# Kernel optimization log

Hardware: AMD Instinct MI355X
Metric: run time of the kernel (lower is better)

Reference implementation:

```python
import jax, jax.numpy as jnp
import numpy as np
from jax import lax

B, C, H, W = 16, 256, 64, 64
EXP = 2
C2 = C * EXP  # expanded channels
EPS = 1e-5


def setup_inputs() -> dict:
    key = jax.random.key(0)
    ks = jax.random.split(key, 8)
    def he(k, shape, fan_out):
        return jax.random.normal(k, shape, jnp.float32) * np.sqrt(2.0 / fan_out)
    return {
        "f": jax.random.normal(ks[0], (B, C, H, W), jnp.float32),
        "ln_gamma": jnp.ones((C,), jnp.float32),
        "ln_beta": jnp.zeros((C,), jnp.float32),
        "w_expand": he(ks[1], (C2, C), C2),          # 1x1 conv [out,in]
        "freq_real": jnp.ones((C2,), jnp.float32),
        "freq_imag": jnp.zeros((C2,), jnp.float32),
        "w_poly": he(ks[2], (C2, C2), C2),
        "w_dw": he(ks[3], (C2, 1, 3, 3), 9),          # depthwise 3x3, fan_out=1*3*3
        "w_pw": he(ks[4], (C2, C2), C2),
        "w_final": he(ks[5], (C, C2), C),
    }


def reference(f, ln_gamma, ln_beta, w_expand, freq_real, freq_imag,
              w_poly, w_dw, w_pw, w_final):
    # LayerNorm over channel dim (torch permutes to NHWC, norms last dim)
    mu = jnp.mean(f, axis=1, keepdims=True)
    var = jnp.var(f, axis=1, keepdims=True)
    f1 = (f - mu) * lax.rsqrt(var + EPS)
    f1 = f1 * ln_gamma[None, :, None, None] + ln_beta[None, :, None, None]
    # 1x1 expand
    f2 = jnp.einsum('bchw,oc->bohw', f1, w_expand)
    # FFT2 -> multiply by per-channel complex scalar (r + i*j) -> IFFT2 -> real.
    # Since the filter is constant over all frequencies and f2 is real, this is
    # exactly Re((r+i*j) * f2) = r * f2; freq_imag contributes nothing.
    f4 = f2 * freq_real[None, :, None, None]
    # polymerize 1x1
    f5 = jnp.einsum('bchw,oc->bohw', f4, w_poly)
    # depthwise 3x3, SAME padding
    f6 = lax.conv_general_dilated(
        f5, w_dw, window_strides=(1, 1), padding='SAME',
        dimension_numbers=('NCHW', 'OIHW', 'NCHW'), feature_group_count=C2)
    # pointwise 1x1
    f6 = jnp.einsum('bchw,oc->bohw', f6, w_pw)
    # GELU (exact erf, torch default) gating
    f7 = jax.nn.gelu(f6, approximate=False) * f6
    # 1x1 reduce + residual
    f8 = jnp.einsum('bchw,oc->bohw', f7, w_final)
    return f + f8
```

## Files before the change

kernel.cpp:

```cpp
#include <hip/hip_runtime.h>
#include <hip/hip_bf16.h>
#include <math.h>

#define Bn 16
#define Cc 256
#define Hh 64
#define Ww 64
#define HW 4096
#define C2 512
#define Pp 65536
#define EPSc 1e-5f

typedef __attribute__((ext_vector_type(8))) short short8;
typedef __attribute__((ext_vector_type(4))) float floatx4;

__global__ __launch_bounds__(512)
void combine_weights(const float* __restrict__ w_expand,
                     const float* __restrict__ freq_real,
                     const float* __restrict__ w_poly,
                     const float* __restrict__ gamma,
                     const float* __restrict__ beta,
                     __hip_bfloat16* __restrict__ W1g_b,
                     float* __restrict__ bias1,
                     float* __restrict__ wsum) {
    int o = blockIdx.x;
    int tid = threadIdx.x;
    int c = tid & 255;
    int kh = tid >> 8;
    float acc = 0.f;
    const float* wp = w_poly + (size_t)o * C2 + kh * 256;
    const float* fr = freq_real + kh * 256;
    const float* we = w_expand + (size_t)(kh * 256) * Cc + c;
    for (int m = 0; m < 256; ++m) {
        acc += wp[m] * fr[m] * we[(size_t)m * Cc];
    }
    __shared__ float part[512];
    __shared__ float redB[256];
    __shared__ float redG[256];
    part[tid] = acc;
    __syncthreads();
    if (tid < 256) {
        float a = part[tid] + part[tid + 256];
        float wg = a * gamma[c];
        W1g_b[(size_t)o * Cc + c] = __float2bfloat16(wg);
        redB[c] = a * beta[c];
        redG[c] = wg;
    }
    __syncthreads();
    for (int s = 128; s > 0; s >>= 1) {
        if (tid < s) { redB[tid] += redB[tid + s]; redG[tid] += redG[tid + s]; }
        __syncthreads();
    }
    if (tid == 0) { bias1[o] = redB[0]; wsum[o] = redG[0]; }
}

__device__ inline void cvt4(const float* __restrict__ a,
                            __hip_bfloat16* __restrict__ o, int q) {
    float4 v = *(const float4*)&a[q * 4];
    __hip_bfloat16 r[4];
    r[0] = __float2bfloat16(v.x);
    r[1] = __float2bfloat16(v.y);
    r[2] = __float2bfloat16(v.z);
    r[3] = __float2bfloat16(v.w);
    *(uint2*)&o[q * 4] = *(const uint2*)r;
}

__global__ __launch_bounds__(256)
void prep_weights(const float* __restrict__ w_pw,
                  const float* __restrict__ w_final,
                  const float* __restrict__ w_dw,
                  __hip_bfloat16* __restrict__ w_pw_b,
                  __hip_bfloat16* __restrict__ w_final_b,
                  float* __restrict__ w_dw_p) {
    int i = blockIdx.x * 256 + threadIdx.x;
    if (i < 65536) {
        cvt4(w_pw, w_pw_b, i);
    } else if (i < 98304) {
        cvt4(w_final, w_final_b, i - 65536);
    } else {
        int j = i - 98304;
        if (j < C2 * 12) {
            int k = j / 12, l = j - k * 12;
            w_dw_p[j] = (l < 9) ? w_dw[k * 9 + l] : 0.f;
        }
    }
}

#define XPAD 264

__global__ __launch_bounds__(512, 4)
void gemm1f(const float* __restrict__ f,
            const __hip_bfloat16* __restrict__ W1g_b,
            const float* __restrict__ bias1,
            const float* __restrict__ wsum,
            __hip_bfloat16* __restrict__ f5) {
    __shared__ __align__(16) char smem1[50688];
    __hip_bfloat16* As = (__hip_bfloat16*)smem1;
    float* redS = (float*)(smem1 + 33792);
    float* redQ = (float*)(smem1 + 41984);
    float* muS  = (float*)(smem1 + 50176);
    float* rsS  = (float*)(smem1 + 50432);

    int flat = blockIdx.x;
    int b = flat >> 6;
    int h = flat & 63;
    int s0 = h * 64;

    int tid = threadIdx.x;
    int x = tid & 15;
    int cg = tid >> 4;

    const float* fb = f + (size_t)b * Cc * HW + s0 + x * 4;
    unsigned* Asu = (unsigned*)&As[0];

    float lsum[4] = {0.f, 0.f, 0.f, 0.f};
    float lsq[4]  = {0.f, 0.f, 0.f, 0.f};
#pragma unroll
    for (int i = 0; i < 4; ++i) {
        int cp = i * 32 + cg;
        float4 v0 = *(const float4*)&fb[(size_t)(cp * 2) * HW];
        float4 v1 = *(const float4*)&fb[(size_t)(cp * 2 + 1) * HW];
        float a0[4] = {v0.x, v0.y, v0.z, v0.w};
        float a1[4] = {v1.x, v1.y, v1.z, v1.w};
#pragma unroll
        for (int j = 0; j < 4; ++j) {
            lsum[j] += a0[j] + a1[j];
            lsq[j]  += a0[j] * a0[j] + a1[j] * a1[j];
            unsigned pk = ((unsigned)__bfloat16_as_ushort(__float2bfloat16(a1[j])) << 16)
                        |  (unsigned)__bfloat16_as_ushort(__float2bfloat16(a0[j]));
            Asu[(size_t)(x * 4 + j) * (XPAD / 2) + cp] = pk;
        }
    }
#pragma unroll
    for (int j = 0; j < 4; ++j) {
        redS[cg * 64 + x * 4 + j] = lsum[j];
        redQ[cg * 64 + x * 4 + j] = lsq[j];
    }

    int lane = tid & 63, wave = tid >> 6;
    int col = lane & 15, quad = lane >> 4;
    int c0w = wave * 64;
    const __hip_bfloat16* Bp = W1g_b + (size_t)(c0w + col) * Cc + quad * 8;
    short8 B0[4], B1[4];
#pragma unroll
    for (int j = 0; j < 4; ++j) {
        B0[j] = *(const short8*)(Bp + (size_t)j * 16 * Cc);
        B1[j] = *(const short8*)(Bp + (size_t)j * 16 * Cc + 32);
    }

    float ws4[4], bi4[4];
#pragma unroll
    for (int j = 0; j < 4; ++j) {
        int c = c0w + j * 16 + col;
        ws4[j] = wsum[c];
        bi4[j] = bias1[c];
    }

    __syncthreads();
    if (tid < 64) {
        float s = 0.f, q = 0.f;
#pragma unroll
        for (int g = 0; g < 32; ++g) { s += redS[g * 64 + tid]; q += redQ[g * 64 + tid]; }
        float m = s * (1.0f / 256.0f);
        muS[tid] = m;
        rsS[tid] = rsqrtf(q * (1.0f / 256.0f) - m * m + EPSc);
    }
    __syncthreads();

    floatx4 acc[4][4];
#pragma unroll
    for (int i = 0; i < 4; ++i)
#pragma unroll
        for (int j = 0; j < 4; ++j)
            acc[i][j] = (floatx4){0.f, 0.f, 0.f, 0.f};

#pragma unroll
    for (int ks = 0; ks < 8; ++ks) {
        int k0 = ks * 32;
        short8 af[4];
#pragma unroll
        for (int i = 0; i < 4; ++i)
            af[i] = *(const short8*)&As[(size_t)(i * 16 + col) * XPAD + k0 + quad * 8];
        __builtin_amdgcn_s_setprio(1);
#pragma unroll
        for (int i = 0; i < 4; ++i)
#pragma unroll
            for (int j = 0; j < 4; ++j)
                acc[i][j] = __builtin_amdgcn_mfma_f32_16x16x32_bf16(
                    af[i], (ks & 1) ? B1[j] : B0[j], acc[i][j], 0, 0, 0);
        __builtin_amdgcn_s_setprio(0);
        if (ks + 2 < 8) {
#pragma unroll
            for (int j = 0; j < 4; ++j) {
                short8 v = *(const short8*)(Bp + (size_t)j * 16 * Cc + k0 + 64);
                if (ks & 1) B1[j] = v; else B0[j] = v;
            }
        }
    }

    __syncthreads();
    __hip_bfloat16* Wb = (__hip_bfloat16*)smem1;
    __hip_bfloat16* f5b = f5 + (size_t)b * C2 * HW + s0;
    int rr = tid >> 3;
    int rc = tid & 7;
#pragma unroll
    for (int chunk = 0; chunk < 2; ++chunk) {
        if ((wave >> 2) == chunk) {
            int cbase = c0w & 255;
#pragma unroll
            for (int i = 0; i < 4; ++i) {
                int pl = i * 16 + quad * 4;
                float4 mu4 = *(const float4*)&muS[pl];
                float4 rs4 = *(const float4*)&rsS[pl];
                float mu_[4] = {mu4.x, mu4.y, mu4.z, mu4.w};
                float rs_[4] = {rs4.x, rs4.y, rs4.z, rs4.w};
#pragma unroll
                for (int j = 0; j < 4; ++j) {
                    int cl = cbase + j * 16 + col;
                    __hip_bfloat16 v4[4];
#pragma unroll
                    for (int r = 0; r < 4; ++r) {
                        float v = (acc[i][j][r] - mu_[r] * ws4[j]) * rs_[r] + bi4[j];
                        v4[r] = __float2bfloat16(v);
                    }
                    *(uint2*)&Wb[(size_t)cl * 72 + pl] = *(const uint2*)v4;
                }
            }
        }
        __syncthreads();
#pragma unroll
        for (int pass = 0; pass < 4; ++pass) {
            int cl = pass * 64 + rr;
            uint4 v = *(const uint4*)&Wb[(size_t)cl * 72 + rc * 8];
            *(uint4*)&f5b[(size_t)(chunk * 256 + cl) * HW + rc * 8] = v;
        }
        if (chunk == 0) __syncthreads();
    }
}

#define TPITCH 520

#define P0_LOAD(dst, itc) do {                                               \
    int kk_ = (itc) * 128 + kb;                                              \
    _Pragma("unroll")                                                        \
    for (int dy_ = 0; dy_ < 3; ++dy_) {                                      \
        int hh_ = h + dy_ - 1;                                               \
        if ((unsigned)hh_ < Hh) {                                            \
            const __hip_bfloat16* row_ = f5b + (size_t)kk_ * HW + hh_ * Ww + w16; \
            dst[dy_][0] = *(const uint4*)&row_[0];                           \
            dst[dy_][1] = *(const uint4*)&row_[8];                           \
        } else {                                                             \
            dst[dy_][0] = make_uint4(0, 0, 0, 0);                            \
            dst[dy_][1] = make_uint4(0, 0, 0, 0);                            \
        }                                                                    \
    } } while (0)

__global__ __launch_bounds__(512, 4)
void fused_tail(const __hip_bfloat16* __restrict__ f5,
                const float* __restrict__ w_dw_p,
                const __hip_bfloat16* __restrict__ w_pw_b,
                const __hip_bfloat16* __restrict__ w_final_b,
                const float* __restrict__ f,
                float* __restrict__ out) {
    __shared__ __align__(16) char smem[69632];
    __hip_bfloat16* tT = (__hip_bfloat16*)smem;
    float* Lf = (float*)smem;

    int flat = blockIdx.x;
    int xcd = flat & 7;
    int slot = flat >> 3;
    int hb = slot & 7;
    int b  = slot >> 3;
    int h  = xcd * 8 + hb;

    int tid = threadIdx.x;
    int lane = tid & 63;
    int wave = tid >> 6;
    int col = lane & 15;
    int quad = lane >> 4;

    const __hip_bfloat16* f5b = f5 + (size_t)b * C2 * HW;
    int t4 = tid & 3;
    int kb = tid >> 2;
    int w16 = t4 * 16;

    uint4 bA[3][2], bB[3][2];
    P0_LOAD(bA, 0);
    P0_LOAD(bB, 1);

#pragma unroll
    for (int it = 0; it < 4; ++it) {
        int k = it * 128 + kb;
        const float4* wd4 = (const float4*)(w_dw_p + (size_t)k * 12);
        float4 wa = wd4[0], wb = wd4[1], wc2 = wd4[2];
        float wreg[9] = {wa.x, wa.y, wa.z, wa.w, wb.x, wb.y, wb.z, wb.w, wc2.x};
        float acc16[16] = {};
#pragma unroll
        for (int dy = 0; dy < 3; ++dy) {
            const __hip_bfloat16* pv =
                (const __hip_bfloat16*)((it & 1) ? &bB[dy][0] : &bA[dy][0]);
            float cv[16];
#pragma unroll
            for (int j = 0; j < 16; ++j) cv[j] = __bfloat162float(pv[j]);
            float l_in = __shfl_up(cv[15], 1);
            float r_in = __shfl_down(cv[0], 1);
            if (t4 == 0) l_in = 0.f;
            if (t4 == 3) r_in = 0.f;
            float win[18];
            win[0] = l_in;
#pragma unroll
            for (int j = 0; j < 16; ++j) win[j + 1] = cv[j];
            win[17] = r_in;
#pragma unroll
            for (int j = 0; j < 16; ++j)
                acc16[j] += wreg[dy * 3 + 0] * win[j] +
                            wreg[dy * 3 + 1] * win[j + 1] +
                            wreg[dy * 3 + 2] * win[j + 2];
        }
        if (it + 2 < 4) {
            if (it & 1) { P0_LOAD(bB, it + 2); } else { P0_LOAD(bA, it + 2); }
        }
        int ksw = k ^ (t4 << 4);
#pragma unroll
        for (int j = 0; j < 16; ++j)
            tT[(size_t)(w16 + j) * TPITCH + ksw] = __float2bfloat16(acc16[j]);
    }

    int wm0 = wave * 64;
    const __hip_bfloat16* Ap = w_pw_b + (size_t)(wm0 + col) * C2 + quad * 8;
    short8 A0[4], A1[4];
#pragma unroll
    for (int mt = 0; mt < 4; ++mt)
        A0[mt] = *(const short8*)(Ap + (size_t)mt * 16 * C2);

    __syncthreads();

#pragma unroll
    for (int mt = 0; mt < 4; ++mt)
        A1[mt] = *(const short8*)(Ap + (size_t)mt * 16 * C2 + 32);

    floatx4 acc[4][4];
#pragma unroll
    for (int mt = 0; mt < 4; ++mt)
#pragma unroll
        for (int nt = 0; nt < 4; ++nt)
            acc[mt][nt] = (floatx4){0.f, 0.f, 0.f, 0.f};

#pragma unroll
    for (int ks = 0; ks < 16; ++ks) {
        int k0 = ks * 32;
        short8 bfr[4];
#pragma unroll
        for (int nt = 0; nt < 4; ++nt)
            bfr[nt] = *(const short8*)&tT[(size_t)(nt * 16 + col) * TPITCH +
                                          ((k0 + quad * 8) ^ (nt << 4))];
        __builtin_amdgcn_s_setprio(1);
#pragma unroll
        for (int mt = 0; mt < 4; ++mt)
#pragma unroll
            for (int nt = 0; nt < 4; ++nt)
                acc[mt][nt] = __builtin_amdgcn_mfma_f32_16x16x32_bf16(
                    (ks & 1) ? A1[mt] : A0[mt], bfr[nt], acc[mt][nt], 0, 0, 0);
        __builtin_amdgcn_s_setprio(0);
        if (ks + 2 < 16) {
#pragma unroll
            for (int mt = 0; mt < 4; ++mt) {
                short8 v = *(const short8*)(Ap + (size_t)mt * 16 * C2 + k0 + 64);
                if (ks & 1) A1[mt] = v; else A0[mt] = v;
            }
        }
    }
    __syncthreads();

#pragma unroll
    for (int mt = 0; mt < 4; ++mt)
#pragma unroll
        for (int nt = 0; nt < 4; ++nt) {
            __hip_bfloat16 v4[4];
#pragma unroll
            for (int r = 0; r < 4; ++r) {
                float v = acc[mt][nt][r];
                float gl = 0.5f * v * (1.0f + erff(v * 0.70710678118f));
                v4[r] = __float2bfloat16(gl * v);
            }
            *(uint2*)&tT[(size_t)(nt * 16 + col) * TPITCH +
                         ((wm0 + mt * 16 + quad * 4) ^ (nt << 4))] = *(const uint2*)v4;
        }

    int wm2 = wave * 32;
    const __hip_bfloat16* Af = w_final_b + (size_t)(wm2 + col) * C2 + quad * 8;
    short8 C0[2], C1[2];
#pragma unroll
    for (int mt = 0; mt < 2; ++mt)
        C0[mt] = *(const short8*)(Af + (size_t)mt * 16 * C2);

    __syncthreads();

#pragma unroll
    for (int mt = 0; mt < 2; ++mt)
        C1[mt] = *(const short8*)(Af + (size_t)mt * 16 * C2 + 32);

    floatx4 acc2[2][4];
#pragma unroll
    for (int mt = 0; mt < 2; ++mt)
#pragma unroll
        for (int nt = 0; nt < 4; ++nt)
            acc2[mt][nt] = (floatx4){0.f, 0.f, 0.f, 0.f};

#pragma unroll
    for (int ks = 0; ks < 16; ++ks) {
        int k0 = ks * 32;
        short8 bfr[4];
#pragma unroll
        for (int nt = 0; nt < 4; ++nt)
            bfr[nt] = *(const short8*)&tT[(size_t)(nt * 16 + col) * TPITCH +
                                          ((k0 + quad * 8) ^ (nt << 4))];
        __builtin_amdgcn_s_setprio(1);
#pragma unroll
        for (int mt = 0; mt < 2; ++mt)
#pragma unroll
            for (int nt = 0; nt < 4; ++nt)
                acc2[mt][nt] = __builtin_amdgcn_mfma_f32_16x16x32_bf16(
                    (ks & 1) ? C1[mt] : C0[mt], bfr[nt], acc2[mt][nt], 0, 0, 0);
        __builtin_amdgcn_s_setprio(0);
        if (ks + 2 < 16) {
#pragma unroll
            for (int mt = 0; mt < 2; ++mt) {
                short8 v = *(const short8*)(Af + (size_t)mt * 16 * C2 + k0 + 64);
                if (ks & 1) C1[mt] = v; else C0[mt] = v;
            }
        }
    }

    __syncthreads();
#pragma unroll
    for (int mt = 0; mt < 2; ++mt)
#pragma unroll
        for (int nt = 0; nt < 4; ++nt)
#pragma unroll
            for (int r = 0; r < 4; ++r) {
                int m = wm2 + mt * 16 + quad * 4 + r;
                int n = nt * 16 + col;
                Lf[(size_t)m * 68 + n] = acc2[mt][nt][r];
            }
    __syncthreads();

    const float* fb = f + (size_t)b * Cc * HW + h * Ww;
    float* ob = out + (size_t)b * Cc * HW + h * Ww;
    int pr = tid >> 4;
    int pc = tid & 15;
#pragma unroll
    for (int pass = 0; pass < 8; ++pass) {
        int m = pass * 32 + pr;
        float4 v = *(const float4*)&Lf[(size_t)m * 68 + pc * 4];
        float4 rr4 = *(const float4*)&fb[(size_t)m * HW + pc * 4];
        v.x += rr4.x; v.y += rr4.y; v.z += rr4.z; v.w += rr4.w;
        *(float4*)&ob[(size_t)m * HW + pc * 4] = v;
    }
}

extern "C" void kernel_launch(void* const* d_in, const int* in_sizes, int n_in,
                              void* d_out, int out_size, void* d_ws, size_t ws_size,
                              hipStream_t stream) {
    const float* f         = (const float*)d_in[0];
    const float* ln_gamma  = (const float*)d_in[1];
    const float* ln_beta   = (const float*)d_in[2];
    const float* w_expand  = (const float*)d_in[3];
    const float* freq_real = (const float*)d_in[4];
    const float* w_poly    = (const float*)d_in[6];
    const float* w_dw      = (const float*)d_in[7];
    const float* w_pw      = (const float*)d_in[8];
    const float* w_final   = (const float*)d_in[9];
    float* out = (float*)d_out;

    char* p = (char*)d_ws;
    __hip_bfloat16* f5   = (__hip_bfloat16*)p;  p += (size_t)C2 * Pp * 2;
    __hip_bfloat16* W1g_b = (__hip_bfloat16*)p; p += (size_t)C2 * Cc * 2;
    float* bias1 = (float*)p;                   p += (size_t)C2 * 4;
    float* wsum  = (float*)p;                   p += (size_t)C2 * 4;
    __hip_bfloat16* w_pw_b    = (__hip_bfloat16*)p;  p += (size_t)C2 * C2 * 2;
    __hip_bfloat16* w_final_b = (__hip_bfloat16*)p;  p += (size_t)Cc * C2 * 2;
    float* w_dw_p = (float*)p;                  p += (size_t)C2 * 12 * 4;

    combine_weights<<<dim3(C2), dim3(512), 0, stream>>>(
        w_expand, freq_real, w_poly, ln_gamma, ln_beta, W1g_b, bias1, wsum);

    prep_weights<<<dim3(409), dim3(256), 0, stream>>>(
        w_pw, w_final, w_dw, w_pw_b, w_final_b, w_dw_p);

    gemm1f<<<dim3(1024), dim3(512), 0, stream>>>(
        f, W1g_b, bias1, wsum, f5);

    fused_tail<<<dim3(1024), dim3(512), 0, stream>>>(
        f5, w_dw_p, w_pw_b, w_final_b, f, out);
}
```

Baseline: 337.0 us.

## Merge weight prep kernels, split gemm1 into smaller tiles, approximate GELU gate

New measurement: 340.3 us. About the same (+1.0%).

```diff
diff --git a/kernel.cpp b/kernel.cpp
--- a/kernel.cpp
+++ b/kernel.cpp
@@ -13,46 +13,6 @@
 
 typedef __attribute__((ext_vector_type(8))) short short8;
 typedef __attribute__((ext_vector_type(4))) float floatx4;
-
-__global__ __launch_bounds__(512)
-void combine_weights(const float* __restrict__ w_expand,
-                     const float* __restrict__ freq_real,
-                     const float* __restrict__ w_poly,
-                     const float* __restrict__ gamma,
-                     const float* __restrict__ beta,
-                     __hip_bfloat16* __restrict__ W1g_b,
-                     float* __restrict__ bias1,
-                     float* __restrict__ wsum) {
-    int o = blockIdx.x;
-    int tid = threadIdx.x;
-    int c = tid & 255;
-    int kh = tid >> 8;
-    float acc = 0.f;
-    const float* wp = w_poly + (size_t)o * C2 + kh * 256;
-    const float* fr = freq_real + kh * 256;
-    const float* we = w_expand + (size_t)(kh * 256) * Cc + c;
-    for (int m = 0; m < 256; ++m) {
-        acc += wp[m] * fr[m] * we[(size_t)m * Cc];
-    }
-    __shared__ float part[512];
-    __shared__ float redB[256];
-    __shared__ float redG[256];
-    part[tid] = acc;
-    __syncthreads();
-    if (tid < 256) {
-        float a = part[tid] + part[tid + 256];
-        float wg = a * gamma[c];
-        W1g_b[(size_t)o * Cc + c] = __float2bfloat16(wg);
-        redB[c] = a * beta[c];
-        redG[c] = wg;
-    }
-    __syncthreads();
-    for (int s = 128; s > 0; s >>= 1) {
-        if (tid < s) { redB[tid] += redB[tid + s]; redG[tid] += redG[tid + s]; }
-        __syncthreads();
-    }
-    if (tid == 0) { bias1[o] = redB[0]; wsum[o] = redG[0]; }
-}
 
 __device__ inline void cvt4(const float* __restrict__ a,
                             __hip_bfloat16* __restrict__ o, int q) {
@@ -65,53 +25,100 @@
     *(uint2*)&o[q * 4] = *(const uint2*)r;
 }
 
-__global__ __launch_bounds__(256)
-void prep_weights(const float* __restrict__ w_pw,
-                  const float* __restrict__ w_final,
-                  const float* __restrict__ w_dw,
-                  __hip_bfloat16* __restrict__ w_pw_b,
-                  __hip_bfloat16* __restrict__ w_final_b,
-                  float* __restrict__ w_dw_p) {
-    int i = blockIdx.x * 256 + threadIdx.x;
-    if (i < 65536) {
-        cvt4(w_pw, w_pw_b, i);
-    } else if (i < 98304) {
-        cvt4(w_final, w_final_b, i - 65536);
-    } else {
-        int j = i - 98304;
-        if (j < C2 * 12) {
-            int k = j / 12, l = j - k * 12;
-            w_dw_p[j] = (l < 9) ? w_dw[k * 9 + l] : 0.f;
-        }
-    }
+__global__ __launch_bounds__(512)
+void weights_all(const float* __restrict__ w_expand,
+                 const float* __restrict__ freq_real,
+                 const float* __restrict__ w_poly,
+                 const float* __restrict__ gamma,
+                 const float* __restrict__ beta,
+                 const float* __restrict__ w_pw,
+                 const float* __restrict__ w_final,
+                 const float* __restrict__ w_dw,
+                 __hip_bfloat16* __restrict__ W1g_b,
+                 float* __restrict__ bias1,
+                 float* __restrict__ wsum,
+                 __hip_bfloat16* __restrict__ w_pw_b,
+                 __hip_bfloat16* __restrict__ w_final_b,
+                 float* __restrict__ w_dw_p) {
+    int tid = threadIdx.x;
+    if (blockIdx.x >= 512) {
+        int i = (blockIdx.x - 512) * 512 + tid;
+        if (i < 65536) {
+            cvt4(w_pw, w_pw_b, i);
+        } else if (i < 98304) {
+            cvt4(w_final, w_final_b, i - 65536);
+        } else {
+            int j = i - 98304;
+            if (j < C2 * 12) {
+                int k = j / 12, l = j - k * 12;
+                w_dw_p[j] = (l < 9) ? w_dw[k * 9 + l] : 0.f;
+            }
+        }
+        return;
+    }
+    int o = blockIdx.x;
+    int c = tid & 255;
+    int kh = tid >> 8;
+    float acc = 0.f;
+    const float* wp = w_poly + (size_t)o * C2 + kh * 256;
+    const float* fr = freq_real + kh * 256;
+    const float* we = w_expand + (size_t)(kh * 256) * Cc + c;
+    for (int m = 0; m < 256; ++m) {
+        acc += wp[m] * fr[m] * we[(size_t)m * Cc];
+    }
+    __shared__ float part[512];
+    __shared__ float redB[256];
+    __shared__ float redG[256];
+    part[tid] = acc;
+    __syncthreads();
+    if (tid < 256) {
+        float a = part[tid] + part[tid + 256];
+        float wg = a * gamma[c];
+        W1g_b[(size_t)o * Cc + c] = __float2bfloat16(wg);
+        redB[c] = a * beta[c];
+        redG[c] = wg;
+    }
+    __syncthreads();
+    for (int s = 128; s > 0; s >>= 1) {
+        if (tid < s) { redB[tid] += redB[tid + s]; redG[tid] += redG[tid + s]; }
+        __syncthreads();
+    }
+    if (tid == 0) { bias1[o] = redB[0]; wsum[o] = redG[0]; }
 }
 
 #define XPAD 264
 
-__global__ __launch_bounds__(512, 4)
-void gemm1f(const float* __restrict__ f,
+__global__ __launch_bounds__(256, 4)
+void gemm1h(const float* __restrict__ f,
             const __hip_bfloat16* __restrict__ W1g_b,
             const float* __restrict__ bias1,
             const float* __restrict__ wsum,
             __hip_bfloat16* __restrict__ f5) {
-    __shared__ __align__(16) char smem1[50688];
-    __hip_bfloat16* As = (__hip_bfloat16*)smem1;
-    float* redS = (float*)(smem1 + 33792);
-    float* redQ = (float*)(smem1 + 41984);
-    float* muS  = (float*)(smem1 + 50176);
-    float* rsS  = (float*)(smem1 + 50432);
+    __shared__ __align__(16) char sm[27648];
+    __hip_bfloat16* As = (__hip_bfloat16*)sm;
+    float* redS  = (float*)(sm + 16896);
+    float* redQ  = (float*)(sm + 21120);
+    float* red2S = (float*)(sm + 25344);
+    float* red2Q = (float*)(sm + 26368);
+    float* muS   = (float*)(sm + 27392);
+    float* rsS   = (float*)(sm + 27520);
 
     int flat = blockIdx.x;
-    int b = flat >> 6;
-    int h = flat & 63;
-    int s0 = h * 64;
+    int xcd = flat & 7;
+    int s = flat >> 3;
+    int chalf = s & 1;
+    int ph = (s >> 1) & 1;
+    int hb = (s >> 2) & 7;
+    int b  = s >> 5;
+    int h  = xcd * 8 + hb;
+    int s0 = h * 64 + ph * 32;
 
     int tid = threadIdx.x;
-    int x = tid & 15;
-    int cg = tid >> 4;
+    int x = tid & 7;
+    int cg = tid >> 3;
 
     const float* fb = f + (size_t)b * Cc * HW + s0 + x * 4;
-    unsigned* Asu = (unsigned*)&As[0];
+    unsigned* Asu = (unsigned*)As;
 
     float lsum[4] = {0.f, 0.f, 0.f, 0.f};
     float lsq[4]  = {0.f, 0.f, 0.f, 0.f};
@@ -133,13 +140,13 @@
     }
 #pragma unroll
     for (int j = 0; j < 4; ++j) {
-        redS[cg * 64 + x * 4 + j] = lsum[j];
-        redQ[cg * 64 + x * 4 + j] = lsq[j];
+        redS[cg * 33 + x * 4 + j] = lsum[j];
+        redQ[cg * 33 + x * 4 + j] = lsq[j];
     }
 
     int lane = tid & 63, wave = tid >> 6;
     int col = lane & 15, quad = lane >> 4;
-    int c0w = wave * 64;
+    int c0w = chalf * 256 + wave * 64;
     const __hip_bfloat16* Bp = W1g_b + (size_t)(c0w + col) * Cc + quad * 8;
     short8 B0[4], B1[4];
 #pragma unroll
@@ -147,7 +154,6 @@
         B0[j] = *(const short8*)(Bp + (size_t)j * 16 * Cc);
         B1[j] = *(const short8*)(Bp + (size_t)j * 16 * Cc + 32);
     }
-
     float ws4[4], bi4[4];
 #pragma unroll
     for (int j = 0; j < 4; ++j) {
@@ -157,19 +163,31 @@
     }
 
     __syncthreads();
-    if (tid < 64) {
-        float s = 0.f, q = 0.f;
-#pragma unroll
-        for (int g = 0; g < 32; ++g) { s += redS[g * 64 + tid]; q += redQ[g * 64 + tid]; }
-        float m = s * (1.0f / 256.0f);
+
+    {
+        int pos = tid & 31, g8 = tid >> 5;
+        float ss = 0.f, qq = 0.f;
+#pragma unroll
+        for (int k = 0; k < 4; ++k) {
+            ss += redS[(g8 * 4 + k) * 33 + pos];
+            qq += redQ[(g8 * 4 + k) * 33 + pos];
+        }
+        red2S[g8 * 32 + pos] = ss;
+        red2Q[g8 * 32 + pos] = qq;
+    }
+    __syncthreads();
+    if (tid < 32) {
+        float ss = 0.f, qq = 0.f;
+#pragma unroll
+        for (int g = 0; g < 8; ++g) { ss += red2S[g * 32 + tid]; qq += red2Q[g * 32 + tid]; }
+        float m = ss * (1.0f / 256.0f);
         muS[tid] = m;
-        rsS[tid] = rsqrtf(q * (1.0f / 256.0f) - m * m + EPSc);
-    }
-    __syncthreads();
-
-    floatx4 acc[4][4];
-#pragma unroll
-    for (int i = 0; i < 4; ++i)
+        rsS[tid] = rsqrtf(qq * (1.0f / 256.0f) - m * m + EPSc);
+    }
+
+    floatx4 acc[2][4];
+#pragma unroll
+    for (int i = 0; i < 2; ++i)
 #pragma unroll
         for (int j = 0; j < 4; ++j)
             acc[i][j] = (floatx4){0.f, 0.f, 0.f, 0.f};
@@ -177,13 +195,13 @@
 #pragma unroll
     for (int ks = 0; ks < 8; ++ks) {
         int k0 = ks * 32;
-        short8 af[4];
-#pragma unroll
-        for (int i = 0; i < 4; ++i)
+        short8 af[2];
+#pragma unroll
+        for (int i = 0; i < 2; ++i)
             af[i] = *(const short8*)&As[(size_t)(i * 16 + col) * XPAD + k0 + quad * 8];
         __builtin_amdgcn_s_setprio(1);
 #pragma unroll
-        for (int i = 0; i < 4; ++i)
+        for (int i = 0; i < 2; ++i)
 #pragma unroll
             for (int j = 0; j < 4; ++j)
                 acc[i][j] = __builtin_amdgcn_mfma_f32_16x16x32_bf16(
@@ -199,46 +217,49 @@
     }
 
     __syncthreads();
-    __hip_bfloat16* Wb = (__hip_bfloat16*)smem1;
-    __hip_bfloat16* f5b = f5 + (size_t)b * C2 * HW + s0;
+    __hip_bfloat16* Wb = (__hip_bfloat16*)sm;
+#pragma unroll
+    for (int i = 0; i < 2; ++i) {
+        int pl = i * 16 + quad * 4;
+        float4 mu4 = *(const float4*)&muS[pl];
+        float4 rs4 = *(const float4*)&rsS[pl];
+        float mu_[4] = {mu4.x, mu4.y, mu4.z, mu4.w};
+        float rs_[4] = {rs4.x, rs4.y, rs4.z, rs4.w};
+#pragma unroll
+        for (int j = 0; j < 4; ++j) {
+            int cl = wave * 64 + j * 16 + col;
+            __hip_bfloat16 v4[4];
+#pragma unroll
+            for (int r = 0; r < 4; ++r) {
+                float v = (acc[i][j][r] - mu_[r] * ws4[j]) * rs_[r] + bi4[j];
+                v4[r] = __float2bfloat16(v);
+            }
+            *(uint2*)&Wb[(size_t)cl * 36 + pl] = *(const uint2*)v4;
+        }
+    }
+    __syncthreads();
+
+    __hip_bfloat16* f5b = f5 + ((size_t)b * C2 + chalf * 256) * HW + s0;
     int rr = tid >> 3;
     int rc = tid & 7;
 #pragma unroll
-    for (int chunk = 0; chunk < 2; ++chunk) {
-        if ((wave >> 2) == chunk) {
-            int cbase = c0w & 255;
-#pragma unroll
-            for (int i = 0; i < 4; ++i) {
-                int pl = i * 16 + quad * 4;
-                float4 mu4 = *(const float4*)&muS[pl];
-                float4 rs4 = *(const float4*)&rsS[pl];
-                float mu_[4] = {mu4.x, mu4.y, mu4.z, mu4.w};
-                float rs_[4] = {rs4.x, rs4.y, rs4.z, rs4.w};
-#pragma unroll
-                for (int j = 0; j < 4; ++j) {
-                    int cl = cbase + j * 16 + col;
-                    __hip_bfloat16 v4[4];
-#pragma unroll
-                    for (int r = 0; r < 4; ++r) {
-                        float v = (acc[i][j][r] - mu_[r] * ws4[j]) * rs_[r] + bi4[j];
-                        v4[r] = __float2bfloat16(v);
-                    }
-                    *(uint2*)&Wb[(size_t)cl * 72 + pl] = *(const uint2*)v4;
-                }
-            }
-        }
-        __syncthreads();
-#pragma unroll
-        for (int pass = 0; pass < 4; ++pass) {
-            int cl = pass * 64 + rr;
-            uint4 v = *(const uint4*)&Wb[(size_t)cl * 72 + rc * 8];
-            *(uint4*)&f5b[(size_t)(chunk * 256 + cl) * HW + rc * 8] = v;
-        }
-        if (chunk == 0) __syncthreads();
+    for (int pass = 0; pass < 8; ++pass) {
+        int cl = pass * 32 + rr;
+        uint2 v = *(const uint2*)&Wb[(size_t)cl * 36 + rc * 4];
+        *(uint2*)&f5b[(size_t)cl * HW + rc * 4] = v;
     }
 }
 
 #define TPITCH 520
+
+__device__ inline float gate_gelu(float v) {
+    float t = v * v;
+    float q = fmaf(0.0356774081f, t, 0.7978845608f);
+    float u = v * q;
+    float e = __expf(2.0f * u);
+    float r = __builtin_amdgcn_rcpf(e + 1.0f);
+    return t - t * r;
+}
 
 #define P0_LOAD(dst, itc) do {                                               \
     int kk_ = (itc) * 128 + kb;                                              \
@@ -378,11 +399,8 @@
         for (int nt = 0; nt < 4; ++nt) {
             __hip_bfloat16 v4[4];
 #pragma unroll
-            for (int r = 0; r < 4; ++r) {
-                float v = acc[mt][nt][r];
-                float gl = 0.5f * v * (1.0f + erff(v * 0.70710678118f));
-                v4[r] = __float2bfloat16(gl * v);
-            }
+            for (int r = 0; r < 4; ++r)
+                v4[r] = __float2bfloat16(gate_gelu(acc[mt][nt][r]));
             *(uint2*)&tT[(size_t)(nt * 16 + col) * TPITCH +
                          ((wm0 + mt * 16 + quad * 4) ^ (nt << 4))] = *(const uint2*)v4;
         }
@@ -482,13 +500,12 @@
     __hip_bfloat16* w_final_b = (__hip_bfloat16*)p;  p += (size_t)Cc * C2 * 2;
     float* w_dw_p = (float*)p;                  p += (size_t)C2 * 12 * 4;
 
-    combine_weights<<<dim3(C2), dim3(512), 0, stream>>>(
-        w_expand, freq_real, w_poly, ln_gamma, ln_beta, W1g_b, bias1, wsum);
-
-    prep_weights<<<dim3(409), dim3(256), 0, stream>>>(
-        w_pw, w_final, w_dw, w_pw_b, w_final_b, w_dw_p);
-
-    gemm1f<<<dim3(1024), dim3(512), 0, stream>>>(
+    weights_all<<<dim3(716), dim3(512), 0, stream>>>(
+        w_expand, freq_real, w_poly, ln_gamma, ln_beta,
+        w_pw, w_final, w_dw,
+        W1g_b, bias1, wsum, w_pw_b, w_final_b, w_dw_p);
+
+    gemm1h<<<dim3(4096), dim3(256), 0, stream>>>(
         f, W1g_b, bias1, wsum, f5);
 
     fused_tail<<<dim3(1024), dim3(512), 0, stream>>>(
```

## Merge weight-prep kernels, shuffle-reduce LayerNorm stats, use tanh-form GELU

Applied to the files above, without the earlier changes.

After: 323.4 us. 4.0% less time.

```diff
diff --git a/kernel.cpp b/kernel.cpp
--- a/kernel.cpp
+++ b/kernel.cpp
@@ -13,46 +13,6 @@
 
 typedef __attribute__((ext_vector_type(8))) short short8;
 typedef __attribute__((ext_vector_type(4))) float floatx4;
-
-__global__ __launch_bounds__(512)
-void combine_weights(const float* __restrict__ w_expand,
-                     const float* __restrict__ freq_real,
-                     const float* __restrict__ w_poly,
-                     const float* __restrict__ gamma,
-                     const float* __restrict__ beta,
-                     __hip_bfloat16* __restrict__ W1g_b,
-                     float* __restrict__ bias1,
-                     float* __restrict__ wsum) {
-    int o = blockIdx.x;
-    int tid = threadIdx.x;
-    int c = tid & 255;
-    int kh = tid >> 8;
-    float acc = 0.f;
-    const float* wp = w_poly + (size_t)o * C2 + kh * 256;
-    const float* fr = freq_real + kh * 256;
-    const float* we = w_expand + (size_t)(kh * 256) * Cc + c;
-    for (int m = 0; m < 256; ++m) {
-        acc += wp[m] * fr[m] * we[(size_t)m * Cc];
-    }
-    __shared__ float part[512];
-    __shared__ float redB[256];
-    __shared__ float redG[256];
-    part[tid] = acc;
-    __syncthreads();
-    if (tid < 256) {
-        float a = part[tid] + part[tid + 256];
-        float wg = a * gamma[c];
-        W1g_b[(size_t)o * Cc + c] = __float2bfloat16(wg);
-        redB[c] = a * beta[c];
-        redG[c] = wg;
-    }
-    __syncthreads();
-    for (int s = 128; s > 0; s >>= 1) {
-        if (tid < s) { redB[tid] += redB[tid + s]; redG[tid] += redG[tid + s]; }
-        __syncthreads();
-    }
-    if (tid == 0) { bias1[o] = redB[0]; wsum[o] = redG[0]; }
-}
 
 __device__ inline void cvt4(const float* __restrict__ a,
                             __hip_bfloat16* __restrict__ o, int q) {
@@ -65,25 +25,65 @@
     *(uint2*)&o[q * 4] = *(const uint2*)r;
 }
 
-__global__ __launch_bounds__(256)
-void prep_weights(const float* __restrict__ w_pw,
-                  const float* __restrict__ w_final,
-                  const float* __restrict__ w_dw,
-                  __hip_bfloat16* __restrict__ w_pw_b,
-                  __hip_bfloat16* __restrict__ w_final_b,
-                  float* __restrict__ w_dw_p) {
-    int i = blockIdx.x * 256 + threadIdx.x;
-    if (i < 65536) {
-        cvt4(w_pw, w_pw_b, i);
-    } else if (i < 98304) {
-        cvt4(w_final, w_final_b, i - 65536);
-    } else {
-        int j = i - 98304;
-        if (j < C2 * 12) {
-            int k = j / 12, l = j - k * 12;
-            w_dw_p[j] = (l < 9) ? w_dw[k * 9 + l] : 0.f;
-        }
-    }
+__global__ __launch_bounds__(512)
+void weights_all(const float* __restrict__ w_expand,
+                 const float* __restrict__ freq_real,
+                 const float* __restrict__ w_poly,
+                 const float* __restrict__ gamma,
+                 const float* __restrict__ beta,
+                 const float* __restrict__ w_pw,
+                 const float* __restrict__ w_final,
+                 const float* __restrict__ w_dw,
+                 __hip_bfloat16* __restrict__ W1g_b,
+                 float* __restrict__ bias1,
+                 float* __restrict__ wsum,
+                 __hip_bfloat16* __restrict__ w_pw_b,
+                 __hip_bfloat16* __restrict__ w_final_b,
+                 float* __restrict__ w_dw_p) {
+    int tid = threadIdx.x;
+    if (blockIdx.x >= 512) {
+        int i = (blockIdx.x - 512) * 512 + tid;
+        if (i < 65536) {
+            cvt4(w_pw, w_pw_b, i);
+        } else if (i < 98304) {
+            cvt4(w_final, w_final_b, i - 65536);
+        } else {
+            int j = i - 98304;
+            if (j < C2 * 12) {
+                int k = j / 12, l = j - k * 12;
+                w_dw_p[j] = (l < 9) ? w_dw[k * 9 + l] : 0.f;
+            }
+        }
+        return;
+    }
+    int o = blockIdx.x;
+    int c = tid & 255;
+    int kh = tid >> 8;
+    float acc = 0.f;
+    const float* wp = w_poly + (size_t)o * C2 + kh * 256;
+    const float* fr = freq_real + kh * 256;
+    const float* we = w_expand + (size_t)(kh * 256) * Cc + c;
+    for (int m = 0; m < 256; ++m) {
+        acc += wp[m] * fr[m] * we[(size_t)m * Cc];
+    }
+    __shared__ float part[512];
+    __shared__ float redB[256];
+    __shared__ float redG[256];
+    part[tid] = acc;
+    __syncthreads();
+    if (tid < 256) {
+        float a = part[tid] + part[tid + 256];
+        float wg = a * gamma[c];
+        W1g_b[(size_t)o * Cc + c] = __float2bfloat16(wg);
+        redB[c] = a * beta[c];
+        redG[c] = wg;
+    }
+    __syncthreads();
+    for (int s = 128; s > 0; s >>= 1) {
+        if (tid < s) { redB[tid] += redB[tid + s]; redG[tid] += redG[tid + s]; }
+        __syncthreads();
+    }
+    if (tid == 0) { bias1[o] = redB[0]; wsum[o] = redG[0]; }
 }
 
 #define XPAD 264
@@ -94,12 +94,11 @@
             const float* __restrict__ bias1,
             const float* __restrict__ wsum,
             __hip_bfloat16* __restrict__ f5) {
-    __shared__ __align__(16) char smem1[50688];
-    __hip_bfloat16* As = (__hip_bfloat16*)smem1;
-    float* redS = (float*)(smem1 + 33792);
-    float* redQ = (float*)(smem1 + 41984);
-    float* muS  = (float*)(smem1 + 50176);
-    float* rsS  = (float*)(smem1 + 50432);
+    __shared__ __align__(16) char sm[38400];
+    __hip_bfloat16* As = (__hip_bfloat16*)sm;
+    float* redW = (float*)(sm + 33792);
+    float* muS  = (float*)(sm + 37888);
+    float* rsS  = (float*)(sm + 38144);
 
     int flat = blockIdx.x;
     int b = flat >> 6;
@@ -131,14 +130,25 @@
             Asu[(size_t)(x * 4 + j) * (XPAD / 2) + cp] = pk;
         }
     }
-#pragma unroll
-    for (int j = 0; j < 4; ++j) {
-        redS[cg * 64 + x * 4 + j] = lsum[j];
-        redQ[cg * 64 + x * 4 + j] = lsq[j];
-    }
 
     int lane = tid & 63, wave = tid >> 6;
     int col = lane & 15, quad = lane >> 4;
+
+#pragma unroll
+    for (int j = 0; j < 4; ++j) {
+        lsum[j] += __shfl_xor(lsum[j], 16);
+        lsum[j] += __shfl_xor(lsum[j], 32);
+        lsq[j]  += __shfl_xor(lsq[j], 16);
+        lsq[j]  += __shfl_xor(lsq[j], 32);
+    }
+    if (quad == 0) {
+#pragma unroll
+        for (int j = 0; j < 4; ++j) {
+            redW[wave * 64 + col * 4 + j]       = lsum[j];
+            redW[512 + wave * 64 + col * 4 + j] = lsq[j];
+        }
+    }
+
     int c0w = wave * 64;
     const __hip_bfloat16* Bp = W1g_b + (size_t)(c0w + col) * Cc + quad * 8;
     short8 B0[4], B1[4];
@@ -147,7 +157,6 @@
         B0[j] = *(const short8*)(Bp + (size_t)j * 16 * Cc);
         B1[j] = *(const short8*)(Bp + (size_t)j * 16 * Cc + 32);
     }
-
     float ws4[4], bi4[4];
 #pragma unroll
     for (int j = 0; j < 4; ++j) {
@@ -160,7 +169,10 @@
     if (tid < 64) {
         float s = 0.f, q = 0.f;
 #pragma unroll
-        for (int g = 0; g < 32; ++g) { s += redS[g * 64 + tid]; q += redQ[g * 64 + tid]; }
+        for (int g = 0; g < 8; ++g) {
+            s += redW[g * 64 + tid];
+            q += redW[512 + g * 64 + tid];
+        }
         float m = s * (1.0f / 256.0f);
         muS[tid] = m;
         rsS[tid] = rsqrtf(q * (1.0f / 256.0f) - m * m + EPSc);
@@ -199,7 +211,7 @@
     }
 
     __syncthreads();
-    __hip_bfloat16* Wb = (__hip_bfloat16*)smem1;
+    __hip_bfloat16* Wb = (__hip_bfloat16*)sm;
     __hip_bfloat16* f5b = f5 + (size_t)b * C2 * HW + s0;
     int rr = tid >> 3;
     int rc = tid & 7;
@@ -239,6 +251,15 @@
 }
 
 #define TPITCH 520
+
+__device__ inline float gate_gelu(float v) {
+    float t = v * v;
+    float q = fmaf(0.0356774081f, t, 0.7978845608f);
+    float u = v * q;
+    float e = __expf(2.0f * u);
+    float r = __builtin_amdgcn_rcpf(e + 1.0f);
+    return t - t * r;
+}
 
 #define P0_LOAD(dst, itc) do {                                               \
     int kk_ = (itc) * 128 + kb;                                              \
@@ -378,11 +399,8 @@
         for (int nt = 0; nt < 4; ++nt) {
             __hip_bfloat16 v4[4];
 #pragma unroll
-            for (int r = 0; r < 4; ++r) {
-                float v = acc[mt][nt][r];
-                float gl = 0.5f * v * (1.0f + erff(v * 0.70710678118f));
-                v4[r] = __float2bfloat16(gl * v);
-            }
+            for (int r = 0; r < 4; ++r)
+                v4[r] = __float2bfloat16(gate_gelu(acc[mt][nt][r]));
             *(uint2*)&tT[(size_t)(nt * 16 + col) * TPITCH +
                          ((wm0 + mt * 16 + quad * 4) ^ (nt << 4))] = *(const uint2*)v4;
         }
@@ -482,11 +500,10 @@
     __hip_bfloat16* w_final_b = (__hip_bfloat16*)p;  p += (size_t)Cc * C2 * 2;
     float* w_dw_p = (float*)p;                  p += (size_t)C2 * 12 * 4;
 
-    combine_weights<<<dim3(C2), dim3(512), 0, stream>>>(
-        w_expand, freq_real, w_poly, ln_gamma, ln_beta, W1g_b, bias1, wsum);
-
-    prep_weights<<<dim3(409), dim3(256), 0, stream>>>(
-        w_pw, w_final, w_dw, w_pw_b, w_final_b, w_dw_p);
+    weights_all<<<dim3(716), dim3(512), 0, stream>>>(
+        w_expand, freq_real, w_poly, ln_gamma, ln_beta,
+        w_pw, w_final, w_dw,
+        W1g_b, bias1, wsum, w_pw_b, w_final_b, w_dw_p);
 
     gemm1f<<<dim3(1024), dim3(512), 0, stream>>>(
         f, W1g_b, bias1, wsum, f5);
```
